# Optimization experiments

Measured on AMD Instinct MI355X. Metric: run time of the kernel, lower is better.

Reference implementation:

```python
import jax, jax.numpy as jnp
import numpy as np


def exp_mix_frac(p1, p2, a1, b1, a2, b2):
    # stable merge of two (numerator, denominator) pairs carried in log-scale p
    p = jnp.maximum(p1, p2)
    e1 = jnp.exp(p1 - p)
    e2 = jnp.exp(p2 - p)
    return a1 * e1 + a2 * e2, b1 * e1 + b2 * e2, p


def assoc_reduce_step(left, right):
    akv_l, ak_l, w_l, p_l = left
    akv_r, ak_r, w_r, p_r = right
    a, b, p = exp_mix_frac(p_l + w_r, p_r, akv_l, ak_l, akv_r, ak_r)
    return a, b, w_l + w_r, p


def setup_inputs() -> dict:
    key = jax.random.key(0)
    ks = jax.random.split(key, 7)
    S, B, E = 2048, 8, 1024
    scale = 1.0 / np.sqrt(E)
    return {
        "x": jax.random.normal(ks[0], (S, B, E), jnp.float32),
        "tmrkv": jax.random.uniform(ks[1], (3 * E,), jnp.float32),
        "Wk": jax.random.normal(ks[2], (E, E), jnp.float32) * scale,
        "Wv": jax.random.normal(ks[3], (E, E), jnp.float32) * scale,
        "time_decay": jax.random.normal(ks[4], (E,), jnp.float32) - 1.0,
        "time_first": jax.random.normal(ks[5], (E,), jnp.float32),
        "Wout": jax.random.normal(ks[6], (E, E), jnp.float32) * scale,
    }


def reference(x, tmrkv, Wk, Wv, time_decay, time_first, Wout):
    # x: (S, B, E) time-major (batch_first=False path of the source module)
    S, B, E = x.shape
    x_prev = jnp.concatenate([jnp.zeros_like(x[:1]), x[:-1]], axis=0)
    # time_mix_rkv layout: [r | k | v]; r-branch is computed in the source but
    # never used in the associative-scan path, so it is omitted (same output).
    mk = tmrkv[E:2 * E]
    mv = tmrkv[2 * E:]
    k = (mk * x + (1.0 - mk) * x_prev) @ Wk  # (S, B, E)
    v = (mv * x + (1.0 - mv) * x_prev) @ Wv  # (S, B, E)

    k_ = k.reshape(S, B * E)
    v_ = v.reshape(S, B * E)
    W_ = jnp.broadcast_to(jnp.tile(time_decay, B)[None, :], (S, B * E))
    ones = jnp.ones_like(v_)
    # log-depth parallel scan over time with numerically-stable exp merge
    a_, b_, _, p_ = jax.lax.associative_scan(
        assoc_reduce_step, (v_, ones, W_, k_), axis=0)

    a_state = a_.reshape(S, B, E)
    b_state = b_.reshape(S, B, E)
    p_state = p_.reshape(S, B, E)
    c, d, _ = exp_mix_frac(p_state, k + time_first + time_decay,
                           a_state, b_state, v, jnp.ones_like(v))
    rwkv = c / d  # (S, B, E)
    return rwkv @ Wout
```

## Files before the change

### kernel.cpp

```cpp
#include <hip/hip_runtime.h>
#include <stdint.h>

#define S_LEN  2048
#define B_DIM  8
#define E_DIM  1024
#define BE     (B_DIM * E_DIM)
#define M_ROWS (S_LEN * B_DIM)
#define NCHUNK 64
#define CLEN   (S_LEN / NCHUNK)

typedef __attribute__((ext_vector_type(8))) short bf16x8;
typedef __attribute__((ext_vector_type(4))) float f32x4;

__device__ __forceinline__ unsigned short f2bf(float f) {
    unsigned int u = __float_as_uint(f);
    u += 0x7FFFu + ((u >> 16) & 1u);
    return (unsigned short)(u >> 16);
}
__device__ __forceinline__ float bf_lo(unsigned int u) {
    return __uint_as_float(u << 16);
}
__device__ __forceinline__ float bf_hi(unsigned int u) {
    return __uint_as_float(u & 0xFFFF0000u);
}

__global__ __launch_bounds__(256) void mix_kernel(
    const float* __restrict__ x, const float* __restrict__ tmrkv,
    unsigned short* __restrict__ xk, unsigned short* __restrict__ xv)
{
    int i = blockIdx.x * 256 + threadIdx.x;
    const float4* x4 = (const float4*)x;
    float4 xc[2], xp[2];
    xc[0] = x4[2 * i];
    xc[1] = x4[2 * i + 1];
    if (i >= BE / 8) {
        xp[0] = x4[2 * i - BE / 4];
        xp[1] = x4[2 * i + 1 - BE / 4];
    } else {
        xp[0] = make_float4(0.f, 0.f, 0.f, 0.f);
        xp[1] = make_float4(0.f, 0.f, 0.f, 0.f);
    }
    int e4 = (2 * i) & (E_DIM / 4 - 1);
    ushort4 ok[2], ov[2];
    #pragma unroll
    for (int h = 0; h < 2; ++h) {
        float4 mk = ((const float4*)(tmrkv + E_DIM))[e4 + h];
        float4 mv = ((const float4*)(tmrkv + 2 * E_DIM))[e4 + h];
        ok[h].x = f2bf(mk.x * xc[h].x + (1.f - mk.x) * xp[h].x);
        ok[h].y = f2bf(mk.y * xc[h].y + (1.f - mk.y) * xp[h].y);
        ok[h].z = f2bf(mk.z * xc[h].z + (1.f - mk.z) * xp[h].z);
        ok[h].w = f2bf(mk.w * xc[h].w + (1.f - mk.w) * xp[h].w);
        ov[h].x = f2bf(mv.x * xc[h].x + (1.f - mv.x) * xp[h].x);
        ov[h].y = f2bf(mv.y * xc[h].y + (1.f - mv.y) * xp[h].y);
        ov[h].z = f2bf(mv.z * xc[h].z + (1.f - mv.z) * xp[h].z);
        ov[h].w = f2bf(mv.w * xc[h].w + (1.f - mv.w) * xp[h].w);
    }
    ((ushort4*)xk)[2 * i]     = ok[0];
    ((ushort4*)xk)[2 * i + 1] = ok[1];
    ((ushort4*)xv)[2 * i]     = ov[0];
    ((ushort4*)xv)[2 * i + 1] = ov[1];
}

__global__ __launch_bounds__(256) void cast_transpose_k(
    const float* __restrict__ w0, const float* __restrict__ w1,
    const float* __restrict__ w2,
    unsigned short* __restrict__ o0, unsigned short* __restrict__ o1,
    unsigned short* __restrict__ o2)
{
    const float* in = blockIdx.z == 0 ? w0 : (blockIdx.z == 1 ? w1 : w2);
    unsigned short* out = blockIdx.z == 0 ? o0 : (blockIdx.z == 1 ? o1 : o2);
    __shared__ float tile[32][33];
    int bx = blockIdx.x * 32, by = blockIdx.y * 32;
    int tx = threadIdx.x, ty = threadIdx.y;
    #pragma unroll
    for (int i = 0; i < 32; i += 8)
        tile[ty + i][tx] = in[(size_t)(by + ty + i) * E_DIM + bx + tx];
    __syncthreads();
    #pragma unroll
    for (int i = 0; i < 32; i += 8)
        out[(size_t)(bx + ty + i) * E_DIM + by + tx] = f2bf(tile[tx][ty + i]);
}

#define BM 128
#define BN 128
#define BK 64

template <typename OutT>
__device__ __forceinline__ void gemm_body(
    const unsigned short* __restrict__ A,
    const unsigned short* __restrict__ BT,
    OutT* __restrict__ C, int M, int N, int K)
{
    __shared__ __align__(16) unsigned short As[BM * BK];
    __shared__ __align__(16) unsigned short Bs[BN * BK];
    const int tid  = threadIdx.x;
    const int wave = tid >> 6, lane = tid & 63;
    const int bm = blockIdx.x * BM, bn = blockIdx.y * BN;
    const int wr = (wave >> 1) * 64, wc = (wave & 1) * 64;
    const int lrow = lane & 15, lq = lane >> 4;

    f32x4 acc[4][4];
    #pragma unroll
    for (int i = 0; i < 4; ++i)
        #pragma unroll
        for (int j = 0; j < 4; ++j)
            acc[i][j] = (f32x4){0.f, 0.f, 0.f, 0.f};

    const int nk = K / BK;
    for (int kt = 0; kt < nk; ++kt) {
        __syncthreads();
        const int kk = kt * BK;
        #pragma unroll
        for (int s = 0; s < 4; ++s) {
            int idx = s * 256 + wave * 64 + lane;
            int r   = idx >> 3;
            int gc  = (idx & 7) ^ (r & 7);
            const char* ga = (const char*)(A  + (size_t)(bm + r) * K + kk) + gc * 16;
            const char* gb = (const char*)(BT + (size_t)(bn + r) * K + kk) + gc * 16;
            char* la = (char*)As + s * 4096 + wave * 1024;
            char* lb = (char*)Bs + s * 4096 + wave * 1024;
            __builtin_amdgcn_global_load_lds(
                (const __attribute__((address_space(1))) unsigned int*)ga,
                (__attribute__((address_space(3))) unsigned int*)la, 16, 0, 0);
            __builtin_amdgcn_global_load_lds(
                (const __attribute__((address_space(1))) unsigned int*)gb,
                (__attribute__((address_space(3))) unsigned int*)lb, 16, 0, 0);
        }
        __syncthreads();

        #pragma unroll
        for (int h = 0; h < 2; ++h) {
            bf16x8 af[4], bf[4];
            #pragma unroll
            for (int i = 0; i < 4; ++i) {
                int R = wr + i * 16 + lrow;
                af[i] = *(const bf16x8*)&As[R * BK + (((h << 2) | lq) ^ (R & 7)) * 8];
            }
            #pragma unroll
            for (int j = 0; j < 4; ++j) {
                int R = wc + j * 16 + lrow;
                bf[j] = *(const bf16x8*)&Bs[R * BK + (((h << 2) | lq) ^ (R & 7)) * 8];
            }
            #pragma unroll
            for (int i = 0; i < 4; ++i)
                #pragma unroll
                for (int j = 0; j < 4; ++j)
                    acc[i][j] = __builtin_amdgcn_mfma_f32_16x16x32_bf16(
                        af[i], bf[j], acc[i][j], 0, 0, 0);
        }
    }

    #pragma unroll
    for (int i = 0; i < 4; ++i)
        #pragma unroll
        for (int j = 0; j < 4; ++j)
            #pragma unroll
            for (int r = 0; r < 4; ++r) {
                int row = bm + wr + i * 16 + lq * 4 + r;
                int col = bn + wc + j * 16 + lrow;
                if constexpr (sizeof(OutT) == 2)
                    C[(size_t)row * N + col] = f2bf(acc[i][j][r]);
                else
                    C[(size_t)row * N + col] = acc[i][j][r];
            }
}

__global__ __launch_bounds__(256) void gemm_kv(
    const unsigned short* __restrict__ A0, const unsigned short* __restrict__ B0,
    unsigned short* __restrict__ C0,
    const unsigned short* __restrict__ A1, const unsigned short* __restrict__ B1,
    unsigned short* __restrict__ C1, int M, int N, int K)
{
    if (blockIdx.z == 0) gemm_body<unsigned short>(A0, B0, C0, M, N, K);
    else                 gemm_body<unsigned short>(A1, B1, C1, M, N, K);
}

__global__ __launch_bounds__(256) void gemm_out(
    const unsigned short* __restrict__ A, const unsigned short* __restrict__ BT,
    float* __restrict__ C, int M, int N, int K)
{
    gemm_body<float>(A, BT, C, M, N, K);
}

__device__ __forceinline__ void wkv_step(float& a, float& b, float& p,
                                         float kt, float vt, float w)
{
    float pw = p + w;
    float pn = fmaxf(pw, kt);
    float e1 = __expf(pw - pn), e2 = __expf(kt - pn);
    a = a * e1 + vt * e2;
    b = b * e1 + e2;
    p = pn;
}

#define Q_PER_T (BE / 4)

__global__ __launch_bounds__(256) void scan_pass1(
    const uint2* __restrict__ k4, const uint2* __restrict__ v4,
    const float* __restrict__ tdec,
    float4* __restrict__ sA, float4* __restrict__ sB, float4* __restrict__ sP)
{
    int g = blockIdx.x * 256 + threadIdx.x;
    int q = g & (Q_PER_T - 1);
    int c = g >> 11;
    float4 w4 = ((const float4*)tdec)[q & (E_DIM / 4 - 1)];
    size_t idx = (size_t)c * CLEN * Q_PER_T + q;
    uint2 ku = k4[idx], vu = v4[idx];
    float a0 = bf_lo(vu.x), b0 = 1.f, p0 = bf_lo(ku.x);
    float a1 = bf_hi(vu.x), b1 = 1.f, p1 = bf_hi(ku.x);
    float a2 = bf_lo(vu.y), b2 = 1.f, p2 = bf_lo(ku.y);
    float a3 = bf_hi(vu.y), b3 = 1.f, p3 = bf_hi(ku.y);
    for (int j = 1; j < CLEN; ++j) {
        idx += Q_PER_T;
        ku = k4[idx]; vu = v4[idx];
        wkv_step(a0, b0, p0, bf_lo(ku.x), bf_lo(vu.x), w4.x);
        wkv_step(a1, b1, p1, bf_hi(ku.x), bf_hi(vu.x), w4.y);
        wkv_step(a2, b2, p2, bf_lo(ku.y), bf_lo(vu.y), w4.z);
        wkv_step(a3, b3, p3, bf_hi(ku.y), bf_hi(vu.y), w4.w);
    }
    sA[g] = make_float4(a0, a1, a2, a3);
    sB[g] = make_float4(b0, b1, b2, b3);
    sP[g] = make_float4(p0, p1, p2, p3);
}

__global__ __launch_bounds__(256) void scan_pass2(
    const float* __restrict__ tdec,
    float* __restrict__ sA, float* __restrict__ sB, float* __restrict__ sP)
{
    __shared__ float tA[64 * 65], tB[64 * 65], tP[64 * 65];
    const int t   = threadIdx.x;
    const int ch0 = blockIdx.x * 64;
    const int chl = t & 63;
    const int cq  = t >> 6;
    #pragma unroll 4
    for (int cc = 0; cc < 16; ++cc) {
        int c = cq * 16 + cc;
        int idx = c * BE + ch0 + chl;
        tA[chl * 65 + c] = sA[idx];
        tB[chl * 65 + c] = sB[idx];
        tP[chl * 65 + c] = sP[idx];
    }
    __syncthreads();
    const int lane = t & 63, wave = t >> 6;
    for (int i = 0; i < 16; ++i) {
        int ch = wave * 16 + i;
        float w = tdec[(ch0 + ch) & (E_DIM - 1)];
        float a = tA[ch * 65 + lane];
        float b = tB[ch * 65 + lane];
        float p = tP[ch * 65 + lane];
        float W = (float)CLEN * w;
        #pragma unroll
        for (int d = 1; d < 64; d <<= 1) {
            float a_l = __shfl_up(a, d);
            float b_l = __shfl_up(b, d);
            float p_l = __shfl_up(p, d);
            float W_l = __shfl_up(W, d);
            if (lane >= d) {
                float pw = p_l + W;
                float pn = fmaxf(pw, p);
                float e1 = __expf(pw - pn), e2 = __expf(p - pn);
                a = a_l * e1 + a * e2;
                b = b_l * e1 + b * e2;
                p = pn;
                W = W_l + W;
            }
        }
        float ea = __shfl_up(a, 1);
        float eb = __shfl_up(b, 1);
        float ep = __shfl_up(p, 1);
        if (lane == 0) { ea = 0.f; eb = 0.f; ep = -__builtin_inff(); }
        tA[ch * 65 + lane] = ea;
        tB[ch * 65 + lane] = eb;
        tP[ch * 65 + lane] = ep;
    }
    __syncthreads();
    #pragma unroll 4
    for (int cc = 0; cc < 16; ++cc) {
        int c = cq * 16 + cc;
        int idx = c * BE + ch0 + chl;
        sA[idx] = tA[chl * 65 + c];
        sB[idx] = tB[chl * 65 + c];
        sP[idx] = tP[chl * 65 + c];
    }
}

__global__ __launch_bounds__(256) void scan_pass3(
    const uint2* __restrict__ k4, const uint2* __restrict__ v4,
    const float* __restrict__ tdec, const float* __restrict__ tfir,
    const float4* __restrict__ sA, const float4* __restrict__ sB,
    const float4* __restrict__ sP, uint2* __restrict__ rwkv4)
{
    int g = blockIdx.x * 256 + threadIdx.x;
    int q = g & (Q_PER_T - 1);
    int c = g >> 11;
    int e4 = q & (E_DIM / 4 - 1);
    float4 w4 = ((const float4*)tdec)[e4];
    float4 f4 = ((const float4*)tfir)[e4];
    float u0 = f4.x + w4.x, u1 = f4.y + w4.y;
    float u2 = f4.z + w4.z, u3 = f4.w + w4.w;
    float4 av = sA[g], bv = sB[g], pv = sP[g];
    float a0 = av.x, b0 = bv.x, p0 = pv.x;
    float a1 = av.y, b1 = bv.y, p1 = pv.y;
    float a2 = av.z, b2 = bv.z, p2 = pv.z;
    float a3 = av.w, b3 = bv.w, p3 = pv.w;
    size_t idx = (size_t)c * CLEN * Q_PER_T + q;
    for (int j = 0; j < CLEN; ++j) {
        uint2 ku = k4[idx], vu = v4[idx];
        float kt0 = bf_lo(ku.x), vt0 = bf_lo(vu.x);
        float kt1 = bf_hi(ku.x), vt1 = bf_hi(vu.x);
        float kt2 = bf_lo(ku.y), vt2 = bf_lo(vu.y);
        float kt3 = bf_hi(ku.y), vt3 = bf_hi(vu.y);
        wkv_step(a0, b0, p0, kt0, vt0, w4.x);
        wkv_step(a1, b1, p1, kt1, vt1, w4.y);
        wkv_step(a2, b2, p2, kt2, vt2, w4.z);
        wkv_step(a3, b3, p3, kt3, vt3, w4.w);
        float kb0 = kt0 + u0, kb1 = kt1 + u1, kb2 = kt2 + u2, kb3 = kt3 + u3;
        float q0 = fmaxf(p0, kb0), q1 = fmaxf(p1, kb1);
        float q2 = fmaxf(p2, kb2), q3 = fmaxf(p3, kb3);
        float g0 = __expf(p0 - q0), h0 = __expf(kb0 - q0);
        float g1 = __expf(p1 - q1), h1 = __expf(kb1 - q1);
        float g2 = __expf(p2 - q2), h2 = __expf(kb2 - q2);
        float g3 = __expf(p3 - q3), h3 = __expf(kb3 - q3);
        float r0 = (a0 * g0 + vt0 * h0) / (b0 * g0 + h0);
        float r1 = (a1 * g1 + vt1 * h1) / (b1 * g1 + h1);
        float r2 = (a2 * g2 + vt2 * h2) / (b2 * g2 + h2);
        float r3 = (a3 * g3 + vt3 * h3) / (b3 * g3 + h3);
        uint2 o;
        o.x = (unsigned int)f2bf(r0) | ((unsigned int)f2bf(r1) << 16);
        o.y = (unsigned int)f2bf(r2) | ((unsigned int)f2bf(r3) << 16);
        rwkv4[idx] = o;
        idx += Q_PER_T;
    }
}

extern "C" void kernel_launch(void* const* d_in, const int* in_sizes, int n_in,
                              void* d_out, int out_size, void* d_ws, size_t ws_size,
                              hipStream_t stream)
{
    const float* x     = (const float*)d_in[0];
    const float* tmrkv = (const float*)d_in[1];
    const float* Wk    = (const float*)d_in[2];
    const float* Wv    = (const float*)d_in[3];
    const float* tdec  = (const float*)d_in[4];
    const float* tfir  = (const float*)d_in[5];
    const float* Wout  = (const float*)d_in[6];
    float* out = (float*)d_out;

    char* ws = (char*)d_ws;
    const size_t SZ_BF = (size_t)M_ROWS * E_DIM * 2;
    unsigned short* xk   = (unsigned short*)(ws);
    unsigned short* xv   = (unsigned short*)(ws + SZ_BF);
    unsigned short* kbuf = (unsigned short*)(ws + 2 * SZ_BF);
    unsigned short* vbuf = (unsigned short*)(ws + 3 * SZ_BF);
    unsigned short* WkT  = (unsigned short*)(ws + 4 * SZ_BF);
    unsigned short* WvT  = WkT + (size_t)E_DIM * E_DIM;
    unsigned short* WoutT= WvT + (size_t)E_DIM * E_DIM;
    float* sA = (float*)xv;
    float* sB = sA + (size_t)NCHUNK * BE;
    float* sP = sB + (size_t)NCHUNK * BE;
    unsigned short* rwkv = xk;

    mix_kernel<<<(M_ROWS * E_DIM / 8) / 256, 256, 0, stream>>>(x, tmrkv, xk, xv);

    dim3 tb(32, 8), tg(E_DIM / 32, E_DIM / 32, 3);
    cast_transpose_k<<<tg, tb, 0, stream>>>(Wk, Wv, Wout, WkT, WvT, WoutT);

    dim3 gkv(M_ROWS / BM, E_DIM / BN, 2);
    gemm_kv<<<gkv, 256, 0, stream>>>(xk, WkT, kbuf, xv, WvT, vbuf,
                                     M_ROWS, E_DIM, E_DIM);

    scan_pass1<<<(NCHUNK * Q_PER_T) / 256, 256, 0, stream>>>(
        (const uint2*)kbuf, (const uint2*)vbuf, tdec,
        (float4*)sA, (float4*)sB, (float4*)sP);
    scan_pass2<<<BE / 64, 256, 0, stream>>>(tdec, sA, sB, sP);
    scan_pass3<<<(NCHUNK * Q_PER_T) / 256, 256, 0, stream>>>(
        (const uint2*)kbuf, (const uint2*)vbuf, tdec, tfir,
        (const float4*)sA, (const float4*)sB, (const float4*)sP,
        (uint2*)rwkv);

    dim3 gg(M_ROWS / BM, E_DIM / BN);
    gemm_out<<<gg, 256, 0, stream>>>(rwkv, WoutT, out, M_ROWS, E_DIM, E_DIM);
}
```

Baseline: 330.3 us.

## Use 256x256 double-buffered GEMM tiles with interleaved async LDS staging

Rewrites the bf16 MFMA GEMM body to use 256x256 block tiles with 512 threads, a double-buffered LDS layout split into half-K planes, and staging of the next tile interleaved between MFMA groups using explicit waitcnt and barriers. The aim is to overlap global-to-LDS loads with compute and to increase data reuse per block. The trade-offs are 128 KB of LDS, which limits each CU to one block, and fewer blocks in the grid, which can cause tail or occupancy issues. The hand-tuned waitcnt sequencing is also fragile.

```diff
diff --git a/kernel.cpp b/kernel.cpp
--- a/kernel.cpp
+++ b/kernel.cpp
@@ -81,9 +81,22 @@
         out[(size_t)(bx + ty + i) * E_DIM + by + tx] = f2bf(tile[tx][ty + i]);
 }
 
-#define BM 128
-#define BN 128
+#define BM 256
+#define BN 256
 #define BK 64
+
+__device__ __forceinline__ void stage_plane(unsigned short* lds_base, int buf_plane,
+                                            const unsigned short* gsrc, int K, int wave)
+{
+    #pragma unroll
+    for (int s = 0; s < 2; ++s) {
+        const unsigned short* g = gsrc + (size_t)s * 128 * K;
+        unsigned short* l = lds_base + buf_plane * 8192 + s * 4096 + wave * 512;
+        __builtin_amdgcn_global_load_lds(
+            (const __attribute__((address_space(1))) unsigned int*)g,
+            (__attribute__((address_space(3))) unsigned int*)l, 16, 0, 0);
+    }
+}
 
 template <typename OutT>
 __device__ __forceinline__ void gemm_body(
@@ -91,81 +104,120 @@
     const unsigned short* __restrict__ BT,
     OutT* __restrict__ C, int M, int N, int K)
 {
-    __shared__ __align__(16) unsigned short As[BM * BK];
-    __shared__ __align__(16) unsigned short Bs[BN * BK];
+    __shared__ __align__(16) unsigned short smem[2][4][8192];
     const int tid  = threadIdx.x;
     const int wave = tid >> 6, lane = tid & 63;
+    const int lrow = lane & 15, lq = lane >> 4;
+    const int wm = wave >> 2, wn = wave & 3;
     const int bm = blockIdx.x * BM, bn = blockIdx.y * BN;
-    const int wr = (wave >> 1) * 64, wc = (wave & 1) * 64;
-    const int lrow = lane & 15, lq = lane >> 4;
-
-    f32x4 acc[4][4];
-    #pragma unroll
-    for (int i = 0; i < 4; ++i)
+
+    const int srow = tid >> 2;
+    const int sg   = (tid & 3) ^ ((srow >> 1) & 3);
+    const unsigned short* sAp = A  + (size_t)(bm + srow) * K + sg * 8;
+    const unsigned short* sBp = BT + (size_t)(bn + srow) * K + sg * 8;
+    unsigned short* lb = &smem[0][0][0];
+
+    f32x4 acc[8][4];
+    #pragma unroll
+    for (int i = 0; i < 8; ++i)
         #pragma unroll
         for (int j = 0; j < 4; ++j)
             acc[i][j] = (f32x4){0.f, 0.f, 0.f, 0.f};
 
+    bf16x8 af[4], bfr[4];
+
+#define LDA_(h, ib)                                                           \
+    _Pragma("unroll")                                                         \
+    for (int i = 0; i < 4; ++i) {                                             \
+        int R = wm * 128 + ((ib) + i) * 16 + lrow;                            \
+        af[i] = *(const bf16x8*)&smem[cur][(h) * 2]                           \
+            [R * 32 + ((lq ^ ((R >> 1) & 3)) << 3)];                          \
+    }
+#define LDB_(h)                                                               \
+    _Pragma("unroll")                                                         \
+    for (int j = 0; j < 4; ++j) {                                             \
+        int R = wn * 64 + j * 16 + lrow;                                      \
+        bfr[j] = *(const bf16x8*)&smem[cur][(h) * 2 + 1]                      \
+            [R * 32 + ((lq ^ ((R >> 1) & 3)) << 3)];                          \
+    }
+#define MMA_(ib)                                                              \
+    __builtin_amdgcn_s_setprio(1);                                            \
+    _Pragma("unroll")                                                         \
+    for (int i = 0; i < 4; ++i)                                               \
+        _Pragma("unroll")                                                     \
+        for (int j = 0; j < 4; ++j)                                           \
+            acc[(ib) + i][j] = __builtin_amdgcn_mfma_f32_16x16x32_bf16(       \
+                af[i], bfr[j], acc[(ib) + i][j], 0, 0, 0);                    \
+    __builtin_amdgcn_s_setprio(0);
+
     const int nk = K / BK;
-    for (int kt = 0; kt < nk; ++kt) {
-        __syncthreads();
-        const int kk = kt * BK;
-        #pragma unroll
-        for (int s = 0; s < 4; ++s) {
-            int idx = s * 256 + wave * 64 + lane;
-            int r   = idx >> 3;
-            int gc  = (idx & 7) ^ (r & 7);
-            const char* ga = (const char*)(A  + (size_t)(bm + r) * K + kk) + gc * 16;
-            const char* gb = (const char*)(BT + (size_t)(bn + r) * K + kk) + gc * 16;
-            char* la = (char*)As + s * 4096 + wave * 1024;
-            char* lb = (char*)Bs + s * 4096 + wave * 1024;
-            __builtin_amdgcn_global_load_lds(
-                (const __attribute__((address_space(1))) unsigned int*)ga,
-                (__attribute__((address_space(3))) unsigned int*)la, 16, 0, 0);
-            __builtin_amdgcn_global_load_lds(
-                (const __attribute__((address_space(1))) unsigned int*)gb,
-                (__attribute__((address_space(3))) unsigned int*)lb, 16, 0, 0);
-        }
-        __syncthreads();
-
-        #pragma unroll
-        for (int h = 0; h < 2; ++h) {
-            bf16x8 af[4], bf[4];
-            #pragma unroll
-            for (int i = 0; i < 4; ++i) {
-                int R = wr + i * 16 + lrow;
-                af[i] = *(const bf16x8*)&As[R * BK + (((h << 2) | lq) ^ (R & 7)) * 8];
-            }
-            #pragma unroll
-            for (int j = 0; j < 4; ++j) {
-                int R = wc + j * 16 + lrow;
-                bf[j] = *(const bf16x8*)&Bs[R * BK + (((h << 2) | lq) ^ (R & 7)) * 8];
-            }
-            #pragma unroll
-            for (int i = 0; i < 4; ++i)
-                #pragma unroll
-                for (int j = 0; j < 4; ++j)
-                    acc[i][j] = __builtin_amdgcn_mfma_f32_16x16x32_bf16(
-                        af[i], bf[j], acc[i][j], 0, 0, 0);
-        }
-    }
-
-    #pragma unroll
-    for (int i = 0; i < 4; ++i)
+    stage_plane(lb, 0, sAp,      K, wave);
+    stage_plane(lb, 1, sBp,      K, wave);
+    stage_plane(lb, 2, sAp + 32, K, wave);
+    stage_plane(lb, 3, sBp + 32, K, wave);
+
+    int cur = 0;
+    for (int t = 0; t < nk - 1; ++t) {
+        const int nxt = cur ^ 1;
+        const unsigned short* nA = sAp + (size_t)(t + 1) * BK;
+        const unsigned short* nB = sBp + (size_t)(t + 1) * BK;
+        stage_plane(lb, nxt * 4 + 0, nA, K, wave);
+        asm volatile("s_waitcnt vmcnt(6)" ::: "memory");
+        __builtin_amdgcn_s_barrier();
+        asm volatile("" ::: "memory");
+        LDA_(0, 0); LDB_(0);
+        MMA_(0);
+        stage_plane(lb, nxt * 4 + 1, nB, K, wave);
+        LDA_(0, 4);
+        MMA_(4);
+        stage_plane(lb, nxt * 4 + 2, nA + 32, K, wave);
+        asm volatile("s_waitcnt vmcnt(6)" ::: "memory");
+        __builtin_amdgcn_s_barrier();
+        asm volatile("" ::: "memory");
+        LDA_(1, 0); LDB_(1);
+        MMA_(0);
+        stage_plane(lb, nxt * 4 + 3, nB + 32, K, wave);
+        LDA_(1, 4);
+        asm volatile("s_waitcnt lgkmcnt(0)" ::: "memory");
+        __builtin_amdgcn_s_barrier();
+        asm volatile("" ::: "memory");
+        MMA_(4);
+        cur = nxt;
+    }
+    asm volatile("s_waitcnt vmcnt(4)" ::: "memory");
+    __builtin_amdgcn_s_barrier();
+    asm volatile("" ::: "memory");
+    LDA_(0, 0); LDB_(0);
+    MMA_(0);
+    LDA_(0, 4);
+    MMA_(4);
+    asm volatile("s_waitcnt vmcnt(0)" ::: "memory");
+    __builtin_amdgcn_s_barrier();
+    asm volatile("" ::: "memory");
+    LDA_(1, 0); LDB_(1);
+    MMA_(0);
+    LDA_(1, 4);
+    MMA_(4);
+
+    #pragma unroll
+    for (int i = 0; i < 8; ++i)
         #pragma unroll
         for (int j = 0; j < 4; ++j)
             #pragma unroll
             for (int r = 0; r < 4; ++r) {
-                int row = bm + wr + i * 16 + lq * 4 + r;
-                int col = bn + wc + j * 16 + lrow;
+                int row = bm + wm * 128 + i * 16 + lq * 4 + r;
+                int col = bn + wn * 64 + j * 16 + lrow;
                 if constexpr (sizeof(OutT) == 2)
                     C[(size_t)row * N + col] = f2bf(acc[i][j][r]);
                 else
                     C[(size_t)row * N + col] = acc[i][j][r];
             }
-}
-
-__global__ __launch_bounds__(256) void gemm_kv(
+#undef LDA_
+#undef LDB_
+#undef MMA_
+}
+
+__global__ __launch_bounds__(512, 2) void gemm_kv(
     const unsigned short* __restrict__ A0, const unsigned short* __restrict__ B0,
     unsigned short* __restrict__ C0,
     const unsigned short* __restrict__ A1, const unsigned short* __restrict__ B1,
@@ -175,7 +227,7 @@
     else                 gemm_body<unsigned short>(A1, B1, C1, M, N, K);
 }
 
-__global__ __launch_bounds__(256) void gemm_out(
+__global__ __launch_bounds__(512, 2) void gemm_out(
     const unsigned short* __restrict__ A, const unsigned short* __restrict__ BT,
     float* __restrict__ C, int M, int N, int K)
 {
@@ -366,7 +418,7 @@
     cast_transpose_k<<<tg, tb, 0, stream>>>(Wk, Wv, Wout, WkT, WvT, WoutT);
 
     dim3 gkv(M_ROWS / BM, E_DIM / BN, 2);
-    gemm_kv<<<gkv, 256, 0, stream>>>(xk, WkT, kbuf, xv, WvT, vbuf,
+    gemm_kv<<<gkv, 512, 0, stream>>>(xk, WkT, kbuf, xv, WvT, vbuf,
                                      M_ROWS, E_DIM, E_DIM);
 
     scan_pass1<<<(NCHUNK * Q_PER_T) / 256, 256, 0, stream>>>(
@@ -379,5 +431,5 @@
         (uint2*)rwkv);
 
     dim3 gg(M_ROWS / BM, E_DIM / BN);
-    gemm_out<<<gg, 256, 0, stream>>>(rwkv, WoutT, out, M_ROWS, E_DIM, E_DIM);
-}
+    gemm_out<<<gg, 512, 0, stream>>>(rwkv, WoutT, out, M_ROWS, E_DIM, E_DIM);
+}
```

Measured after the change: 307.5 us. 6.9% less time.
